# Optimization experiments

Hardware: AMD Instinct MI355X
Metric: run time of the kernel (lower is better)

The kernel has to match this reference:

```python
import jax, jax.numpy as jnp
import numpy as np

CTYPE = jnp.complex64


def coeffs_from_zeros(z):
    """coeff[k] = e_k(-z): expand prod_i (1 - z_i * t) in powers of t.

    Matches the TF coeffs_from_zeros (sum over combinations of prod(-z)).
    z: [n] complex. Returns [n+1] complex, coeff[0] == 1.
    """
    n = z.shape[0]
    c = jnp.zeros((n + 1,), CTYPE).at[0].set(1.0)
    for i in range(n):  # fixed tiny n (filter order), not a data dim
        c = c - z[i] * jnp.concatenate([jnp.zeros((1,), CTYPE), c[:-1]])
    return c


def setup_inputs() -> dict:
    key = jax.random.key(0)
    B, T = 4096, 2048
    x = jax.random.normal(key, (B, T, 1), dtype=jnp.float32)
    gain_ri = jnp.array([1.0, 0.0], dtype=jnp.float32)
    # stable conjugate pole pair (radius 0.95) and zero pair (radius 0.8)
    th_p, th_z = 0.3, 0.6
    poles_ri = jnp.array(
        [[0.95 * np.cos(th_p), 0.95 * np.sin(th_p)],
         [0.95 * np.cos(th_p), -0.95 * np.sin(th_p)]], dtype=jnp.float32)
    zeros_ri = jnp.array(
        [[0.8 * np.cos(th_z), 0.8 * np.sin(th_z)],
         [0.8 * np.cos(th_z), -0.8 * np.sin(th_z)]], dtype=jnp.float32)
    return {"x": x, "gain_ri": gain_ri, "poles_ri": poles_ri, "zeros_ri": zeros_ri}


def reference(x, gain_ri, poles_ri, zeros_ri):
    B, T, _ = x.shape
    gain = (gain_ri[0] + 1j * gain_ri[1]).astype(CTYPE)
    poles = (poles_ri[:, 0] + 1j * poles_ri[:, 1]).astype(CTYPE)
    zeros = (zeros_ri[:, 0] + 1j * zeros_ri[:, 1]).astype(CTYPE)
    n_poles, n_zeros = poles.shape[0], zeros.shape[0]

    # hoisted out of the time loop (constant across steps; same values the TF
    # cell recomputes every step)
    pole_coeffs = coeffs_from_zeros(poles)  # [n_poles+1]
    zero_coeffs = coeffs_from_zeros(zeros)  # [n_zeros+1]
    zero_offset = max(0, n_poles - n_zeros)
    den = pole_coeffs[0]
    safe_den = jnp.where(den == 0, jnp.ones((), CTYPE), den)  # divide_no_nan
    gz = gain * zero_coeffs  # [n_zeros+1]

    def step(carry, xt):
        xm, ym = carry  # real [B, n_poles+1] (TF casts state back to real)
        xmc = jnp.concatenate([xt.astype(CTYPE), xm[:, :-1].astype(CTYPE)], axis=1)
        num = jnp.sum(xmc[:, zero_offset:] * gz, axis=1, keepdims=True)
        num = num - jnp.sum(ym[:, :-1].astype(CTYPE) * pole_coeffs[1:], axis=1,
                            keepdims=True)
        y = jnp.where(den == 0, jnp.zeros((), CTYPE), num / safe_den)
        ymc = jnp.concatenate([y, ym[:, :-1].astype(CTYPE)], axis=1)
        return (jnp.real(xmc), jnp.real(ymc)), jnp.real(y).astype(x.dtype)

    s0 = (jnp.zeros((B, n_poles + 1), x.dtype), jnp.zeros((B, n_poles + 1), x.dtype))
    _, ys = jax.lax.scan(step, s0, jnp.swapaxes(x, 0, 1))  # ys: [T, B, 1]
    return jnp.swapaxes(ys, 0, 1)  # [B, T, 1]
```

## Files before the change

kernel.cpp:

```cpp
#include <hip/hip_runtime.h>


#define T_LEN   2048
#define B_ROWS  4096
#define CHUNK   32
#define LANES   64
#define ROWS_PER_BLOCK 4

__global__ __launch_bounds__(256, 4) void pzcell_scan_kernel(
    const float* __restrict__ x,
    const float* __restrict__ gain_ri,
    const float* __restrict__ poles_ri,
    const float* __restrict__ zeros_ri,
    float* __restrict__ out)
{
    float gr = gain_ri[0], gi = gain_ri[1];
    float p1r = poles_ri[0];
    float p2r = poles_ri[2];
    float p1i = poles_ri[1], p2i = poles_ri[3];
    float z1r = zeros_ri[0], z1i = zeros_ri[1];
    float z2r = zeros_ri[2], z2i = zeros_ri[3];

    float a1 = -(p1r + p2r);
    float a2 = p1r * p2r - p1i * p2i;
    float zc1r = -(z1r + z2r), zc1i = -(z1i + z2i);
    float zc2r = z1r * z2r - z1i * z2i;
    float zc2i = z1r * z2i + z1i * z2r;
    float b0 = gr;
    float b1 = gr * zc1r - gi * zc1i;
    float b2 = gr * zc2r - gi * zc2i;

    int lane = threadIdx.x & 63;
    int wv   = threadIdx.x >> 6;
    int row  = blockIdx.x * ROWS_PER_BLOCK + wv;

    const float* xr = x + (size_t)row * T_LEN + lane * CHUNK;

    float xm1 = 0.f, xm2 = 0.f;
    if (lane > 0) { xm1 = xr[-1]; xm2 = xr[-2]; }

    float4 xv[8];
#pragma unroll
    for (int i = 0; i < 8; ++i) xv[i] = ((const float4*)xr)[i];

    float y[CHUNK];
    float y1 = 0.f, y2 = 0.f;
#pragma unroll
    for (int i = 0; i < 8; ++i) {
        float xi, f, yt;
        xi = xv[i].x;
        f  = b0 * xi + b1 * xm1 + b2 * xm2;
        yt = f - a1 * y1 - a2 * y2;
        y[4 * i + 0] = yt; xm2 = xm1; xm1 = xi; y2 = y1; y1 = yt;

        xi = xv[i].y;
        f  = b0 * xi + b1 * xm1 + b2 * xm2;
        yt = f - a1 * y1 - a2 * y2;
        y[4 * i + 1] = yt; xm2 = xm1; xm1 = xi; y2 = y1; y1 = yt;

        xi = xv[i].z;
        f  = b0 * xi + b1 * xm1 + b2 * xm2;
        yt = f - a1 * y1 - a2 * y2;
        y[4 * i + 2] = yt; xm2 = xm1; xm1 = xi; y2 = y1; y1 = yt;

        xi = xv[i].w;
        f  = b0 * xi + b1 * xm1 + b2 * xm2;
        yt = f - a1 * y1 - a2 * y2;
        y[4 * i + 3] = yt; xm2 = xm1; xm1 = xi; y2 = y1; y1 = yt;
    }

    float m00 = -a1, m01 = -a2, m10 = 1.f, m11 = 0.f;
#pragma unroll
    for (int s = 0; s < 5; ++s) {
        float t00 = m00 * m00 + m01 * m10;
        float t01 = m00 * m01 + m01 * m11;
        float t10 = m10 * m00 + m11 * m10;
        float t11 = m10 * m01 + m11 * m11;
        m00 = t00; m01 = t01; m10 = t10; m11 = t11;
    }

    float v1 = y1, v2 = y2;
    float p00 = m00, p01 = m01, p10 = m10, p11 = m11;
#pragma unroll
    for (int k = 1; k < 64; k <<= 1) {
        float u1 = __shfl_up(v1, (unsigned)k);
        float u2 = __shfl_up(v2, (unsigned)k);
        if (lane < k) { u1 = 0.f; u2 = 0.f; }
        v1 += p00 * u1 + p01 * u2;
        v2 += p10 * u1 + p11 * u2;
        float t00 = p00 * p00 + p01 * p10;
        float t01 = p00 * p01 + p01 * p11;
        float t10 = p10 * p00 + p11 * p10;
        float t11 = p10 * p01 + p11 * p11;
        p00 = t00; p01 = t01; p10 = t10; p11 = t11;
    }

    float s1 = __shfl_up(v1, 1);
    float s2 = __shfl_up(v2, 1);
    if (lane == 0) { s1 = 0.f; s2 = 0.f; }

    float4* yo = (float4*)(out + (size_t)row * T_LEN + lane * CHUNK);
    float c1 = s1, c2 = s2;
#pragma unroll
    for (int i = 0; i < 8; ++i) {
        float4 o; float c;
        c = -a1 * c1 - a2 * c2; o.x = y[4 * i + 0] + c; c2 = c1; c1 = c;
        c = -a1 * c1 - a2 * c2; o.y = y[4 * i + 1] + c; c2 = c1; c1 = c;
        c = -a1 * c1 - a2 * c2; o.z = y[4 * i + 2] + c; c2 = c1; c1 = c;
        c = -a1 * c1 - a2 * c2; o.w = y[4 * i + 3] + c; c2 = c1; c1 = c;
        yo[i] = o;
    }
}

extern "C" void kernel_launch(void* const* d_in, const int* in_sizes, int n_in,
                              void* d_out, int out_size, void* d_ws, size_t ws_size,
                              hipStream_t stream) {
    const float* x        = (const float*)d_in[0];
    const float* gain_ri  = (const float*)d_in[1];
    const float* poles_ri = (const float*)d_in[2];
    const float* zeros_ri = (const float*)d_in[3];
    float* out = (float*)d_out;

    dim3 block(64 * ROWS_PER_BLOCK);
    dim3 grid(B_ROWS / ROWS_PER_BLOCK);
    hipLaunchKernelGGL(pzcell_scan_kernel, grid, block, 0, stream,
                       x, gain_ri, poles_ri, zeros_ri, out);
}
```

Baseline: 95.86 us.

## Stage x loads and y stores through swizzled LDS for coalesced global access

Each wave now loads its row into shared memory with fully coalesced float4 accesses, using an XOR swizzle to avoid bank conflicts. Each lane then reads its contiguous 32-element chunk from LDS, and gets the x history values from the neighbouring lane via a shuffle instead of extra global loads. Outputs are staged back through LDS and written to global memory coalesced. This removes strided per-lane global accesses at the cost of 32KB of LDS per block and extra barriers, which may limit occupancy.

```diff
diff --git a/kernel.cpp b/kernel.cpp
--- a/kernel.cpp
+++ b/kernel.cpp
@@ -4,7 +4,6 @@
 #define T_LEN   2048
 #define B_ROWS  4096
 #define CHUNK   32
-#define LANES   64
 #define ROWS_PER_BLOCK 4
 
 __global__ __launch_bounds__(256, 4) void pzcell_scan_kernel(
@@ -14,6 +13,8 @@
     const float* __restrict__ zeros_ri,
     float* __restrict__ out)
 {
+    __shared__ float lds[ROWS_PER_BLOCK][T_LEN];
+
     float gr = gain_ri[0], gi = gain_ri[1];
     float p1r = poles_ri[0];
     float p2r = poles_ri[2];
@@ -34,14 +35,25 @@
     int wv   = threadIdx.x >> 6;
     int row  = blockIdx.x * ROWS_PER_BLOCK + wv;
 
-    const float* xr = x + (size_t)row * T_LEN + lane * CHUNK;
+    float4* l4 = (float4*)lds[wv];
 
-    float xm1 = 0.f, xm2 = 0.f;
-    if (lane > 0) { xm1 = xr[-1]; xm2 = xr[-2]; }
+    const float4* xg4 = (const float4*)(x + (size_t)row * T_LEN);
+    int swz_g = (lane >> 3) & 7;
+#pragma unroll
+    for (int j = 0; j < 8; ++j) {
+        int g = j * 64 + lane;
+        l4[g ^ swz_g] = xg4[g];
+    }
+    __syncthreads();
 
     float4 xv[8];
+    int qbase = lane * 8, swz_c = lane & 7;
 #pragma unroll
-    for (int i = 0; i < 8; ++i) xv[i] = ((const float4*)xr)[i];
+    for (int k = 0; k < 8; ++k) xv[k] = l4[(qbase + k) ^ swz_c];
+
+    float xm1 = __shfl_up(xv[7].w, 1);
+    float xm2 = __shfl_up(xv[7].z, 1);
+    if (lane == 0) { xm1 = 0.f; xm2 = 0.f; }
 
     float y[CHUNK];
     float y1 = 0.f, y2 = 0.f;
@@ -99,7 +111,7 @@
     float s2 = __shfl_up(v2, 1);
     if (lane == 0) { s1 = 0.f; s2 = 0.f; }
 
-    float4* yo = (float4*)(out + (size_t)row * T_LEN + lane * CHUNK);
+    __syncthreads();
     float c1 = s1, c2 = s2;
 #pragma unroll
     for (int i = 0; i < 8; ++i) {
@@ -108,7 +120,15 @@
         c = -a1 * c1 - a2 * c2; o.y = y[4 * i + 1] + c; c2 = c1; c1 = c;
         c = -a1 * c1 - a2 * c2; o.z = y[4 * i + 2] + c; c2 = c1; c1 = c;
         c = -a1 * c1 - a2 * c2; o.w = y[4 * i + 3] + c; c2 = c1; c1 = c;
-        yo[i] = o;
+        l4[(qbase + i) ^ swz_c] = o;
+    }
+    __syncthreads();
+
+    float4* og4 = (float4*)(out + (size_t)row * T_LEN);
+#pragma unroll
+    for (int j = 0; j < 8; ++j) {
+        int g = j * 64 + lane;
+        og4[g] = l4[g ^ swz_g];
     }
 }
 
```

Result: faster. 86.32 us (-9.9%).
